# Kernel tuning notes

Measured on AMD Instinct MI355X. Metric: run time of the kernel, lower is better.

## Reference

```python
import jax, jax.numpy as jnp
import numpy as np

B, D, H, G, WR = 8192, 1024, 1024, 2, 64
URANKS = [64, 64]


def setup_inputs() -> dict:
    key = jax.random.key(0)
    ks = jax.random.split(key, 12)
    s = 0.1
    return {
        "x": jax.random.normal(ks[0], (B, D), jnp.float32),
        "h": jax.random.normal(ks[1], (B, H), jnp.float32),
        "c": jax.random.normal(ks[2], (B, H), jnp.float32),
        "dia_x": s * jax.random.normal(ks[3], (1, D), jnp.float32),
        "dia_h": s * jax.random.normal(ks[4], (1, H), jnp.float32),
        "Ux": s * jax.random.normal(ks[5], (D, WR), jnp.float32),
        "Vx": s * jax.random.normal(ks[6], (4 * H, WR), jnp.float32),
        "Uh_0": s * jax.random.normal(ks[7], (G, H // G, URANKS[0]), jnp.float32),
        "Vh_0": s * jax.random.normal(ks[8], (G, URANKS[0], 4 * (H // G)), jnp.float32),
        "Uh_1": s * jax.random.normal(ks[9], (G, H // G, URANKS[1]), jnp.float32),
        "Vh_1": s * jax.random.normal(ks[10], (G, URANKS[1], 4 * (H // G)), jnp.float32),
        "bias_x": jnp.ones((1, 4 * H), jnp.float32),
        "bias_h": jnp.ones((1, 4 * H), jnp.float32),
    }


def reference(x, h, c, dia_x, dia_h, Ux, Vx, Uh_0, Vh_0, Uh_1, Vh_1, bias_x, bias_h):
    Bn, Dn = x.shape
    Hn = h.shape[1]
    g = Uh_0.shape[0]
    Hg = Hn // g
    r0 = Uh_0.shape[2]

    # diagonal (vector-multiplication) paths, x-part zero-padded to hidden width
    vm_x = jnp.pad(dia_x * x, ((0, 0), (0, Hn - Dn)))          # [B, H]
    vm_h = dia_h * h                                           # [B, H]

    # low-rank input projection
    lowered_x = (x @ Ux) @ Vx.T                                # [B, 4H]

    # refined diagonal corrections subtracted from the low-rank outputs
    Vx4 = Vx.reshape(4, Hn, -1)[:, :Dn, :]                     # [4, D, wR]
    coef_x = jnp.sum(Ux[None, :, :] * Vx4, axis=-1)            # [4, D]
    vm_refined_x = jnp.pad(x[:, None, :] * coef_x[None], ((0, 0), (0, 0), (0, Hn - Dn))).reshape(Bn, 4 * Hn)

    Uh0f = Uh_0.reshape(Hn, r0)                                # [H, r0]
    Vh0f = jnp.transpose(Vh_0, (0, 2, 1)).reshape(4 * Hn, r0).reshape(4, Hn, r0)
    coef_h = jnp.sum(Uh0f[None, :, :] * Vh0f, axis=-1)         # [4, H]
    vm_refined_h = (h[:, None, :] * coef_h[None]).reshape(Bn, 4 * Hn)

    gx = lowered_x - vm_refined_x + bias_x
    xi, xf, xo, xn = jnp.split(gx, 4, axis=1)

    # grouped low-rank recurrent projection with cyclic group permutation
    hv = h.reshape(Bn, g, Hg)
    Uhs = [Uh_0, Uh_1]
    Vhs = [Vh_0, Vh_1]
    g_h = jnp.zeros((Bn, 4 * Hn), x.dtype)
    for i in range(g):
        idx = np.roll(np.arange(g), -i)                        # static permutation
        hp = hv[:, idx, :]                                     # [B, g, H/g]
        t = jnp.einsum('bgn,gnr->bgr', hp, Uhs[i])             # [B, g, r_i]
        t = jnp.einsum('bgr,grm->bgm', t, Vhs[i])              # [B, g, 4H/g]
        g_h = g_h + t.reshape(Bn, 4 * Hn)

    gh = g_h - vm_refined_h + bias_h
    hf, hi, hn, ho = jnp.split(gh, 4, axis=1)                  # note gate order differs from x

    base = vm_x + vm_h
    inputgate = jax.nn.sigmoid(xi + hi + base)
    forgetgate = jax.nn.sigmoid(xf + hf + base)
    outputgate = jax.nn.sigmoid(xo + ho + base)
    newgate = jnp.tanh(xn + hn + base)

    c_next = forgetgate * c + inputgate * newgate
    h_next = outputgate * jnp.tanh(c_next)
    return (h_next, c_next)
```

## Files before the change

### kernel.cpp

```cpp
#include <hip/hip_runtime.h>


typedef _Float16 half8 __attribute__((ext_vector_type(8)));
typedef _Float16 half4v __attribute__((ext_vector_type(4)));
typedef float f32x4 __attribute__((ext_vector_type(4)));

#define WS_U1F   0
#define WS_UH1F  131072
#define WS_W2    393216
#define WS_CX    1966080
#define WS_CH    1982464
#define WS_BB    1998848

__global__ __launch_bounds__(256) void prep_kernel(
    const float* __restrict__ Ux, const float* __restrict__ Vx,
    const float* __restrict__ Uh0, const float* __restrict__ Vh0,
    const float* __restrict__ Uh1, const float* __restrict__ Vh1,
    const float* __restrict__ dia_x, const float* __restrict__ dia_h,
    const float* __restrict__ bias_x, const float* __restrict__ bias_h,
    _Float16* __restrict__ U1f, _Float16* __restrict__ Uh1f,
    _Float16* __restrict__ W2f, float* __restrict__ cx,
    float* __restrict__ ch, float* __restrict__ bb)
{
    __shared__ __align__(16) _Float16 Tl[64][260];

    const int tid = threadIdx.x;
    if (blockIdx.x >= 240) {
        int bid2 = blockIdx.x - 240;
        int s = bid2 & 1, i = (bid2 >> 1) & 1, mchunk = bid2 >> 2;
        const float* Vh = i ? Vh1 : Vh0;
        #pragma unroll
        for (int it = 0; it < 16; ++it) {
            int idx = tid + it * 256;
            int row = idx >> 6, c4 = idx & 63;
            f32x4 v = *(const f32x4*)&Vh[(size_t)(s * 64 + row) * 2048
                                         + mchunk * 256 + c4 * 4];
            half4v p;
            p[0] = (_Float16)v[0]; p[1] = (_Float16)v[1];
            p[2] = (_Float16)v[2]; p[3] = (_Float16)v[3];
            *(half4v*)&Tl[row][c4 * 4] = p;
        }
        __syncthreads();
        int lane = tid & 63, l15 = lane & 15, quad = lane >> 4;
        #pragma unroll
        for (int q = 0; q < 8; ++q) {
            int combo = (tid >> 6) * 8 + q;
            int ct_local = combo >> 1, rk = combo & 1;
            int m_local = ct_local * 16 + l15;
            int m = mchunk * 256 + m_local;
            int g01 = (m >= 1024) ? 0 : 1;
            int ct_global = (m - (1 - g01) * 1024) >> 4;
            int ksq = 2 + 2 * i + rk;
            half8 v8;
            #pragma unroll
            for (int jj = 0; jj < 8; ++jj)
                v8[jj] = Tl[rk * 32 + quad * 8 + jj][m_local];
            size_t t_out = (((size_t)(s * 2 + g01) * 64 + ct_global) * 6 + ksq) * 64 + lane;
            *(half8*)&W2f[t_out * 8] = v8;
        }
        return;
    }

    int e = blockIdx.x * 256 + tid;
    if (e < 8192) {
        int lane = e & 63, ks = (e >> 6) & 31, ct = e >> 11;
        int l15 = lane & 15, quad = lane >> 4;
        half8 v8;
        #pragma unroll
        for (int jj = 0; jj < 8; ++jj) {
            int k = ks * 32 + quad * 8 + jj;
            v8[jj] = (_Float16)Ux[k * 64 + ct * 16 + l15];
        }
        *(half8*)&U1f[(size_t)e * 8] = v8;
    } else if (e < 24576) {
        int t = e - 8192;
        int lane = t & 63, ks = (t >> 6) & 15, ct = (t >> 10) & 3, j = t >> 12;
        int l15 = lane & 15, quad = lane >> 4;
        const float* src = (j & 1) ? Uh1 : Uh0;
        int g = j >> 1;
        half8 v8;
        #pragma unroll
        for (int jj = 0; jj < 8; ++jj) {
            int k = ks * 32 + quad * 8 + jj;
            v8[jj] = (_Float16)src[(g * 512 + k) * 64 + ct * 16 + l15];
        }
        *(half8*)&Uh1f[(size_t)t * 8] = v8;
    } else if (e < 57344) {
        int tt = e - 24576;
        int lane = tt & 63;
        int ksq2 = (tt >> 6) & 1;
        int ct   = (tt / 128) & 63;
        int g01  = (tt / 8192) & 1;
        int s    = tt / 16384;
        int l15 = lane & 15, quad = lane >> 4;
        int k = ct * 16 + l15;
        int jx = s * 2 + g01;
        half8 v8;
        #pragma unroll
        for (int jj = 0; jj < 8; ++jj) {
            int r = ksq2 * 32 + quad * 8 + jj;
            v8[jj] = (_Float16)Vx[(jx * 1024 + k) * 64 + r];
        }
        size_t t_out = (((size_t)(s * 2 + g01) * 64 + ct) * 6 + ksq2) * 64 + lane;
        *(half8*)&W2f[t_out * 8] = v8;
    } else if (e < 61440) {
        int t = e - 57344;
        int q = t >> 10; int k = t & 1023;
        int jh = q ^ 1;
        int fh = jh * 1024 + k; int g = fh >> 11; int m = fh & 2047;
        float sx0 = 0.f, sx1 = 0.f, sh0 = 0.f, sh1 = 0.f;
        #pragma unroll 4
        for (int r = 0; r < 64; r += 2) {
            sx0 += Ux[k * 64 + r]     * Vx[(q * 1024 + k) * 64 + r];
            sx1 += Ux[k * 64 + r + 1] * Vx[(q * 1024 + k) * 64 + r + 1];
            sh0 += Uh0[k * 64 + r]     * Vh0[(size_t)(g * 64 + r) * 2048 + m];
            sh1 += Uh0[k * 64 + r + 1] * Vh0[(size_t)(g * 64 + r + 1) * 2048 + m];
        }
        cx[t] = dia_x[k] - (sx0 + sx1);
        ch[t] = dia_h[k] - (sh0 + sh1);
        bb[t] = bias_x[q * 1024 + k] + bias_h[jh * 1024 + k];
    }
}

__global__ __launch_bounds__(1024) void fused_kernel(
    const float* __restrict__ x, const float* __restrict__ h,
    const float* __restrict__ c,
    const _Float16* __restrict__ U1f, const _Float16* __restrict__ Uh1f,
    const _Float16* __restrict__ W2f,
    const float* __restrict__ cx, const float* __restrict__ ch,
    const float* __restrict__ bb, float* __restrict__ out)
{
    __shared__ __align__(16) _Float16 Xsh[32][1032];
    __shared__ __align__(16) _Float16 Hsh[32][1032];
    __shared__ __align__(16) _Float16 Tsh[32][328];

    const int tid = threadIdx.x;
    const int w = tid >> 6, l = tid & 63, l15 = l & 15, quad = l >> 4;
    const int b0 = blockIdx.x * 32;
    const size_t rowbase = (size_t)b0 * 1024;

    {
        const float* xs = x + rowbase;
        const float* hs = h + rowbase;
        #pragma unroll
        for (int ii = 0; ii < 8; ++ii) {
            int idx = tid + ii * 1024;
            int row = idx >> 8, c4 = idx & 255;
            f32x4 fx = *(const f32x4*)&xs[(size_t)row * 1024 + c4 * 4];
            f32x4 fh = *(const f32x4*)&hs[(size_t)row * 1024 + c4 * 4];
            half4v px, ph;
            px[0] = (_Float16)fx[0]; px[1] = (_Float16)fx[1];
            px[2] = (_Float16)fx[2]; px[3] = (_Float16)fx[3];
            ph[0] = (_Float16)fh[0]; ph[1] = (_Float16)fh[1];
            ph[2] = (_Float16)fh[2]; ph[3] = (_Float16)fh[3];
            *(half4v*)&Xsh[row][c4 * 4] = px;
            *(half4v*)&Hsh[row][c4 * 4] = ph;
        }
    }
    __syncthreads();

    if (w < 8) {
        int rt = w & 1, ct = w >> 1;
        f32x4 acc = {};
        const _Float16* bp = U1f + ((size_t)(ct * 32) * 64 + l) * 8;
        #pragma unroll
        for (int ks = 0; ks < 32; ++ks) {
            half8 a = *(const half8*)&Xsh[rt * 16 + l15][ks * 32 + quad * 8];
            half8 b = *(const half8*)(bp + (size_t)ks * 512);
            acc = __builtin_amdgcn_mfma_f32_16x16x32_f16(a, b, acc, 0, 0, 0);
        }
        #pragma unroll
        for (int r = 0; r < 4; ++r)
            Tsh[rt * 16 + quad * 4 + r][ct * 16 + l15] = (_Float16)acc[r];
    }
    {
        int pstart = (w < 8) ? w : 8 + (w - 8) * 3;
        int pcnt   = (w < 8) ? 1 : 3;
        for (int ii = 0; ii < 3; ++ii) {
            if (ii >= pcnt) break;
            int p = pstart + ii;
            int j = p >> 3, rem = p & 7, prt = rem >> 2, pct = rem & 3;
            int hoff = (j == 1 || j == 2) ? 512 : 0;
            f32x4 pa = {};
            const _Float16* pb = Uh1f + ((size_t)((j * 4 + pct) * 16) * 64 + l) * 8;
            #pragma unroll
            for (int ks = 0; ks < 16; ++ks) {
                half8 a = *(const half8*)&Hsh[prt * 16 + l15][hoff + ks * 32 + quad * 8];
                half8 b = *(const half8*)(pb + (size_t)ks * 512);
                pa = __builtin_amdgcn_mfma_f32_16x16x32_f16(a, b, pa, 0, 0, 0);
            }
            #pragma unroll
            for (int r = 0; r < 4; ++r)
                Tsh[prt * 16 + quad * 4 + r][64 + j * 64 + pct * 16 + l15] = (_Float16)pa[r];
        }
    }
    __syncthreads();

    const int secIF[3] = {0, 64, 128};
    const int secON[3] = {0, 192, 256};

    float cpref[2][2][4];
    {
        int k0 = w * 16 + l15;
        #pragma unroll
        for (int rt = 0; rt < 2; ++rt)
            #pragma unroll
            for (int r = 0; r < 4; ++r)
                cpref[0][rt][r] = __builtin_nontemporal_load(
                    &c[rowbase + (size_t)(rt * 16 + quad * 4 + r) * 1024 + k0]);
    }

    #pragma unroll
    for (int i = 0; i < 4; ++i) {
        const int ctg = w + 16 * i;
        const int k = ctg * 16 + l15;

        if (i < 3) {
            int kn = k + 256;
            #pragma unroll
            for (int rt = 0; rt < 2; ++rt)
                #pragma unroll
                for (int r = 0; r < 4; ++r)
                    cpref[(i + 1) & 1][rt][r] = __builtin_nontemporal_load(
                        &c[rowbase + (size_t)(rt * 16 + quad * 4 + r) * 1024 + kn]);
        }

        float cxi = cx[k], cxf = cx[1024 + k], cxo = cx[2048 + k], cxn = cx[3072 + k];
        float chi = ch[k], chf = ch[1024 + k], cho = ch[2048 + k], chn = ch[3072 + k];
        float bbi = bb[k], bbf = bb[1024 + k], bbo = bb[2048 + k], bbn = bb[3072 + k];

        const size_t laneoff = (size_t)l * 8;
        const _Float16* bpi = W2f + (size_t)((0 * 64 + ctg) * 6) * 512 + laneoff;
        const _Float16* bpf = W2f + (size_t)((1 * 64 + ctg) * 6) * 512 + laneoff;
        const _Float16* bpo = W2f + (size_t)((2 * 64 + ctg) * 6) * 512 + laneoff;
        const _Float16* bpn = W2f + (size_t)((3 * 64 + ctg) * 6) * 512 + laneoff;

        f32x4 acc[4][2] = {};
        #pragma unroll
        for (int ks = 0; ks < 6; ++ks) {
            half8 bi = *(const half8*)(bpi + (size_t)ks * 512);
            half8 bf = *(const half8*)(bpf + (size_t)ks * 512);
            half8 bo = *(const half8*)(bpo + (size_t)ks * 512);
            half8 bn = *(const half8*)(bpn + (size_t)ks * 512);
            int coff = (ks & 1) * 32 + quad * 8;
            #pragma unroll
            for (int rt = 0; rt < 2; ++rt) {
                half8 aA = *(const half8*)&Tsh[rt * 16 + l15][secIF[ks >> 1] + coff];
                half8 aB = *(const half8*)&Tsh[rt * 16 + l15][secON[ks >> 1] + coff];
                acc[0][rt] = __builtin_amdgcn_mfma_f32_16x16x32_f16(aA, bi, acc[0][rt], 0, 0, 0);
                acc[1][rt] = __builtin_amdgcn_mfma_f32_16x16x32_f16(aA, bf, acc[1][rt], 0, 0, 0);
                acc[2][rt] = __builtin_amdgcn_mfma_f32_16x16x32_f16(aB, bo, acc[2][rt], 0, 0, 0);
                acc[3][rt] = __builtin_amdgcn_mfma_f32_16x16x32_f16(aB, bn, acc[3][rt], 0, 0, 0);
            }
        }

        #pragma unroll
        for (int rt = 0; rt < 2; ++rt) {
            #pragma unroll
            for (int r = 0; r < 4; ++r) {
                int rl = rt * 16 + quad * 4 + r;
                size_t off = rowbase + (size_t)rl * 1024 + k;
                float xv = (float)Xsh[rl][k];
                float hv = (float)Hsh[rl][k];
                float cvv = cpref[i & 1][rt][r];
                float pi = acc[0][rt][r] + xv * cxi + hv * chi + bbi;
                float pf = acc[1][rt][r] + xv * cxf + hv * chf + bbf;
                float po = acc[2][rt][r] + xv * cxo + hv * cho + bbo;
                float pn = acc[3][rt][r] + xv * cxn + hv * chn + bbn;
                float ig = __builtin_amdgcn_rcpf(1.f + __expf(-pi));
                float fg = __builtin_amdgcn_rcpf(1.f + __expf(-pf));
                float og = __builtin_amdgcn_rcpf(1.f + __expf(-po));
                float ng = 1.f - 2.f * __builtin_amdgcn_rcpf(__expf(2.f * pn) + 1.f);
                float cn = fg * cvv + ig * ng;
                float tc = 1.f - 2.f * __builtin_amdgcn_rcpf(__expf(2.f * cn) + 1.f);
                out[off] = og * tc;
                out[(size_t)8388608 + off] = cn;
            }
        }
    }
}

extern "C" void kernel_launch(void* const* d_in, const int* in_sizes, int n_in,
                              void* d_out, int out_size, void* d_ws, size_t ws_size,
                              hipStream_t stream)
{
    const float* x      = (const float*)d_in[0];
    const float* h      = (const float*)d_in[1];
    const float* c      = (const float*)d_in[2];
    const float* dia_x  = (const float*)d_in[3];
    const float* dia_h  = (const float*)d_in[4];
    const float* Ux     = (const float*)d_in[5];
    const float* Vx     = (const float*)d_in[6];
    const float* Uh0    = (const float*)d_in[7];
    const float* Vh0    = (const float*)d_in[8];
    const float* Uh1    = (const float*)d_in[9];
    const float* Vh1    = (const float*)d_in[10];
    const float* bias_x = (const float*)d_in[11];
    const float* bias_h = (const float*)d_in[12];
    float* out = (float*)d_out;

    char* ws = (char*)d_ws;
    _Float16* U1f  = (_Float16*)(ws + WS_U1F);
    _Float16* Uh1f = (_Float16*)(ws + WS_UH1F);
    _Float16* W2f  = (_Float16*)(ws + WS_W2);
    float* cx = (float*)(ws + WS_CX);
    float* ch = (float*)(ws + WS_CH);
    float* bb = (float*)(ws + WS_BB);

    prep_kernel<<<272, 256, 0, stream>>>(Ux, Vx, Uh0, Vh0, Uh1, Vh1,
                                         dia_x, dia_h, bias_x, bias_h,
                                         U1f, Uh1f, W2f, cx, ch, bb);
    fused_kernel<<<256, 1024, 0, stream>>>(x, h, c, U1f, Uh1f, W2f,
                                           cx, ch, bb, out);
}
```

Baseline: 215.0 us.

## Merge weight prep and fused LSTM kernel into one cooperative launch

Combines the weight-repacking prep kernel and the main fused LSTM-cell kernel into a single cooperative kernel with a grid-wide sync. The first blocks do the repacking while every block loads and converts its x/h tile to fp16 in shared memory, and a grid barrier separates the phases. This removes one kernel launch and lets the x/h loads overlap with weight preparation. In exchange it needs all 256 blocks of 1024 threads to be co-resident, and it adds the cost of a grid-wide barrier.

```diff
diff --git a/kernel.cpp b/kernel.cpp
--- a/kernel.cpp
+++ b/kernel.cpp
@@ -1,4 +1,7 @@
 #include <hip/hip_runtime.h>
+#include <hip/hip_cooperative_groups.h>
+
+namespace cg = cooperative_groups;
 
 
 typedef _Float16 half8 __attribute__((ext_vector_type(8)));
@@ -12,132 +15,129 @@
 #define WS_CH    1982464
 #define WS_BB    1998848
 
-__global__ __launch_bounds__(256) void prep_kernel(
+#define XSH(r,c) POOL[(r) * 1032 + (c)]
+#define HSH(r,c) POOL[33024 + (r) * 1032 + (c)]
+#define TSH(r,c) POOL[66048 + (r) * 328 + (c)]
+
+__global__ __launch_bounds__(1024) void mega_kernel(
+    const float* __restrict__ x, const float* __restrict__ h,
+    const float* __restrict__ c,
+    const float* __restrict__ dia_x, const float* __restrict__ dia_h,
     const float* __restrict__ Ux, const float* __restrict__ Vx,
     const float* __restrict__ Uh0, const float* __restrict__ Vh0,
     const float* __restrict__ Uh1, const float* __restrict__ Vh1,
-    const float* __restrict__ dia_x, const float* __restrict__ dia_h,
     const float* __restrict__ bias_x, const float* __restrict__ bias_h,
     _Float16* __restrict__ U1f, _Float16* __restrict__ Uh1f,
     _Float16* __restrict__ W2f, float* __restrict__ cx,
-    float* __restrict__ ch, float* __restrict__ bb)
+    float* __restrict__ ch, float* __restrict__ bb,
+    float* __restrict__ out)
 {
-    __shared__ __align__(16) _Float16 Tl[64][260];
+    __shared__ __align__(16) _Float16 POOL[76544];
 
     const int tid = threadIdx.x;
-    if (blockIdx.x >= 240) {
-        int bid2 = blockIdx.x - 240;
-        int s = bid2 & 1, i = (bid2 >> 1) & 1, mchunk = bid2 >> 2;
-        const float* Vh = i ? Vh1 : Vh0;
+    const int bid = blockIdx.x;
+    const int w = tid >> 6, l = tid & 63, l15 = l & 15, quad = l >> 4;
+    const int b0 = bid * 32;
+    const size_t rowbase = (size_t)b0 * 1024;
+
+    if (bid < 8) {
+        int unit = tid >> 8;
+        int ut   = tid & 255;
+        int bid2 = bid * 4 + unit;
+        _Float16* Tl = POOL + unit * 16640;
+        int s = bid2 & 1, ih = (bid2 >> 1) & 1, mchunk = bid2 >> 2;
+        const float* Vh = ih ? Vh1 : Vh0;
         #pragma unroll
         for (int it = 0; it < 16; ++it) {
-            int idx = tid + it * 256;
+            int idx = ut + it * 256;
             int row = idx >> 6, c4 = idx & 63;
             f32x4 v = *(const f32x4*)&Vh[(size_t)(s * 64 + row) * 2048
                                          + mchunk * 256 + c4 * 4];
             half4v p;
             p[0] = (_Float16)v[0]; p[1] = (_Float16)v[1];
             p[2] = (_Float16)v[2]; p[3] = (_Float16)v[3];
-            *(half4v*)&Tl[row][c4 * 4] = p;
+            *(half4v*)&Tl[row * 260 + c4 * 4] = p;
         }
         __syncthreads();
-        int lane = tid & 63, l15 = lane & 15, quad = lane >> 4;
+        int lane = ut & 63, tl15 = lane & 15, tquad = lane >> 4;
         #pragma unroll
         for (int q = 0; q < 8; ++q) {
-            int combo = (tid >> 6) * 8 + q;
+            int combo = (ut >> 6) * 8 + q;
             int ct_local = combo >> 1, rk = combo & 1;
-            int m_local = ct_local * 16 + l15;
+            int m_local = ct_local * 16 + tl15;
             int m = mchunk * 256 + m_local;
             int g01 = (m >= 1024) ? 0 : 1;
             int ct_global = (m - (1 - g01) * 1024) >> 4;
-            int ksq = 2 + 2 * i + rk;
+            int ksq = 2 + 2 * ih + rk;
             half8 v8;
             #pragma unroll
             for (int jj = 0; jj < 8; ++jj)
-                v8[jj] = Tl[rk * 32 + quad * 8 + jj][m_local];
+                v8[jj] = Tl[(rk * 32 + tquad * 8 + jj) * 260 + m_local];
             size_t t_out = (((size_t)(s * 2 + g01) * 64 + ct_global) * 6 + ksq) * 64 + lane;
             *(half8*)&W2f[t_out * 8] = v8;
         }
-        return;
-    }
-
-    int e = blockIdx.x * 256 + tid;
-    if (e < 8192) {
-        int lane = e & 63, ks = (e >> 6) & 31, ct = e >> 11;
-        int l15 = lane & 15, quad = lane >> 4;
-        half8 v8;
-        #pragma unroll
-        for (int jj = 0; jj < 8; ++jj) {
-            int k = ks * 32 + quad * 8 + jj;
-            v8[jj] = (_Float16)Ux[k * 64 + ct * 16 + l15];
-        }
-        *(half8*)&U1f[(size_t)e * 8] = v8;
-    } else if (e < 24576) {
-        int t = e - 8192;
-        int lane = t & 63, ks = (t >> 6) & 15, ct = (t >> 10) & 3, j = t >> 12;
-        int l15 = lane & 15, quad = lane >> 4;
-        const float* src = (j & 1) ? Uh1 : Uh0;
-        int g = j >> 1;
-        half8 v8;
-        #pragma unroll
-        for (int jj = 0; jj < 8; ++jj) {
-            int k = ks * 32 + quad * 8 + jj;
-            v8[jj] = (_Float16)src[(g * 512 + k) * 64 + ct * 16 + l15];
-        }
-        *(half8*)&Uh1f[(size_t)t * 8] = v8;
-    } else if (e < 57344) {
-        int tt = e - 24576;
-        int lane = tt & 63;
-        int ksq2 = (tt >> 6) & 1;
-        int ct   = (tt / 128) & 63;
-        int g01  = (tt / 8192) & 1;
-        int s    = tt / 16384;
-        int l15 = lane & 15, quad = lane >> 4;
-        int k = ct * 16 + l15;
-        int jx = s * 2 + g01;
-        half8 v8;
-        #pragma unroll
-        for (int jj = 0; jj < 8; ++jj) {
-            int r = ksq2 * 32 + quad * 8 + jj;
-            v8[jj] = (_Float16)Vx[(jx * 1024 + k) * 64 + r];
-        }
-        size_t t_out = (((size_t)(s * 2 + g01) * 64 + ct) * 6 + ksq2) * 64 + lane;
-        *(half8*)&W2f[t_out * 8] = v8;
-    } else if (e < 61440) {
-        int t = e - 57344;
-        int q = t >> 10; int k = t & 1023;
-        int jh = q ^ 1;
-        int fh = jh * 1024 + k; int g = fh >> 11; int m = fh & 2047;
-        float sx0 = 0.f, sx1 = 0.f, sh0 = 0.f, sh1 = 0.f;
-        #pragma unroll 4
-        for (int r = 0; r < 64; r += 2) {
-            sx0 += Ux[k * 64 + r]     * Vx[(q * 1024 + k) * 64 + r];
-            sx1 += Ux[k * 64 + r + 1] * Vx[(q * 1024 + k) * 64 + r + 1];
-            sh0 += Uh0[k * 64 + r]     * Vh0[(size_t)(g * 64 + r) * 2048 + m];
-            sh1 += Uh0[k * 64 + r + 1] * Vh0[(size_t)(g * 64 + r + 1) * 2048 + m];
-        }
-        cx[t] = dia_x[k] - (sx0 + sx1);
-        ch[t] = dia_h[k] - (sh0 + sh1);
-        bb[t] = bias_x[q * 1024 + k] + bias_h[jh * 1024 + k];
-    }
-}
-
-__global__ __launch_bounds__(1024) void fused_kernel(
-    const float* __restrict__ x, const float* __restrict__ h,
-    const float* __restrict__ c,
-    const _Float16* __restrict__ U1f, const _Float16* __restrict__ Uh1f,
-    const _Float16* __restrict__ W2f,
-    const float* __restrict__ cx, const float* __restrict__ ch,
-    const float* __restrict__ bb, float* __restrict__ out)
-{
-    __shared__ __align__(16) _Float16 Xsh[32][1032];
-    __shared__ __align__(16) _Float16 Hsh[32][1032];
-    __shared__ __align__(16) _Float16 Tsh[32][328];
-
-    const int tid = threadIdx.x;
-    const int w = tid >> 6, l = tid & 63, l15 = l & 15, quad = l >> 4;
-    const int b0 = blockIdx.x * 32;
-    const size_t rowbase = (size_t)b0 * 1024;
+    } else if (bid < 68) {
+        int e = (bid - 8) * 1024 + tid;
+        if (e < 8192) {
+            int lane = e & 63, ks = (e >> 6) & 31, ct = e >> 11;
+            int pl15 = lane & 15, pquad = lane >> 4;
+            half8 v8;
+            #pragma unroll
+            for (int jj = 0; jj < 8; ++jj) {
+                int k = ks * 32 + pquad * 8 + jj;
+                v8[jj] = (_Float16)Ux[k * 64 + ct * 16 + pl15];
+            }
+            *(half8*)&U1f[(size_t)e * 8] = v8;
+        } else if (e < 24576) {
+            int t = e - 8192;
+            int lane = t & 63, ks = (t >> 6) & 15, ct = (t >> 10) & 3, j = t >> 12;
+            int pl15 = lane & 15, pquad = lane >> 4;
+            const float* src = (j & 1) ? Uh1 : Uh0;
+            int g = j >> 1;
+            half8 v8;
+            #pragma unroll
+            for (int jj = 0; jj < 8; ++jj) {
+                int k = ks * 32 + pquad * 8 + jj;
+                v8[jj] = (_Float16)src[(g * 512 + k) * 64 + ct * 16 + pl15];
+            }
+            *(half8*)&Uh1f[(size_t)t * 8] = v8;
+        } else if (e < 57344) {
+            int tt = e - 24576;
+            int lane = tt & 63;
+            int ksq2 = (tt >> 6) & 1;
+            int ct   = (tt / 128) & 63;
+            int g01  = (tt / 8192) & 1;
+            int s    = tt / 16384;
+            int pl15 = lane & 15, pquad = lane >> 4;
+            int k = ct * 16 + pl15;
+            int jx = s * 2 + g01;
+            half8 v8;
+            #pragma unroll
+            for (int jj = 0; jj < 8; ++jj) {
+                int r = ksq2 * 32 + pquad * 8 + jj;
+                v8[jj] = (_Float16)Vx[(jx * 1024 + k) * 64 + r];
+            }
+            size_t t_out = (((size_t)(s * 2 + g01) * 64 + ct) * 6 + ksq2) * 64 + lane;
+            *(half8*)&W2f[t_out * 8] = v8;
+        } else {
+            int t = e - 57344;
+            int q = t >> 10; int k = t & 1023;
+            int jh = q ^ 1;
+            int fh = jh * 1024 + k; int g = fh >> 11; int m = fh & 2047;
+            float sx0 = 0.f, sx1 = 0.f, sh0 = 0.f, sh1 = 0.f;
+            #pragma unroll 4
+            for (int r = 0; r < 64; r += 2) {
+                sx0 += Ux[k * 64 + r]     * Vx[(q * 1024 + k) * 64 + r];
+                sx1 += Ux[k * 64 + r + 1] * Vx[(q * 1024 + k) * 64 + r + 1];
+                sh0 += Uh0[k * 64 + r]     * Vh0[(size_t)(g * 64 + r) * 2048 + m];
+                sh1 += Uh0[k * 64 + r + 1] * Vh0[(size_t)(g * 64 + r + 1) * 2048 + m];
+            }
+            cx[t] = dia_x[k] - (sx0 + sx1);
+            ch[t] = dia_h[k] - (sh0 + sh1);
+            bb[t] = bias_x[q * 1024 + k] + bias_h[jh * 1024 + k];
+        }
+    }
+    __syncthreads();
 
     {
         const float* xs = x + rowbase;
@@ -153,11 +153,13 @@
             px[2] = (_Float16)fx[2]; px[3] = (_Float16)fx[3];
             ph[0] = (_Float16)fh[0]; ph[1] = (_Float16)fh[1];
             ph[2] = (_Float16)fh[2]; ph[3] = (_Float16)fh[3];
-            *(half4v*)&Xsh[row][c4 * 4] = px;
-            *(half4v*)&Hsh[row][c4 * 4] = ph;
+            *(half4v*)&XSH(row, c4 * 4) = px;
+            *(half4v*)&HSH(row, c4 * 4) = ph;
         }
     }
     __syncthreads();
+
+    cg::this_grid().sync();
 
     if (w < 8) {
         int rt = w & 1, ct = w >> 1;
@@ -165,13 +167,13 @@
         const _Float16* bp = U1f + ((size_t)(ct * 32) * 64 + l) * 8;
         #pragma unroll
         for (int ks = 0; ks < 32; ++ks) {
-            half8 a = *(const half8*)&Xsh[rt * 16 + l15][ks * 32 + quad * 8];
+            half8 a = *(const half8*)&XSH(rt * 16 + l15, ks * 32 + quad * 8);
             half8 b = *(const half8*)(bp + (size_t)ks * 512);
             acc = __builtin_amdgcn_mfma_f32_16x16x32_f16(a, b, acc, 0, 0, 0);
         }
         #pragma unroll
         for (int r = 0; r < 4; ++r)
-            Tsh[rt * 16 + quad * 4 + r][ct * 16 + l15] = (_Float16)acc[r];
+            TSH(rt * 16 + quad * 4 + r, ct * 16 + l15) = (_Float16)acc[r];
     }
     {
         int pstart = (w < 8) ? w : 8 + (w - 8) * 3;
@@ -185,13 +187,13 @@
             const _Float16* pb = Uh1f + ((size_t)((j * 4 + pct) * 16) * 64 + l) * 8;
             #pragma unroll
             for (int ks = 0; ks < 16; ++ks) {
-                half8 a = *(const half8*)&Hsh[prt * 16 + l15][hoff + ks * 32 + quad * 8];
+                half8 a = *(const half8*)&HSH(prt * 16 + l15, hoff + ks * 32 + quad * 8);
                 half8 b = *(const half8*)(pb + (size_t)ks * 512);
                 pa = __builtin_amdgcn_mfma_f32_16x16x32_f16(a, b, pa, 0, 0, 0);
             }
             #pragma unroll
             for (int r = 0; r < 4; ++r)
-                Tsh[prt * 16 + quad * 4 + r][64 + j * 64 + pct * 16 + l15] = (_Float16)pa[r];
+                TSH(prt * 16 + quad * 4 + r, 64 + j * 64 + pct * 16 + l15) = (_Float16)pa[r];
         }
     }
     __syncthreads();
@@ -245,8 +247,8 @@
             int coff = (ks & 1) * 32 + quad * 8;
             #pragma unroll
             for (int rt = 0; rt < 2; ++rt) {
-                half8 aA = *(const half8*)&Tsh[rt * 16 + l15][secIF[ks >> 1] + coff];
-                half8 aB = *(const half8*)&Tsh[rt * 16 + l15][secON[ks >> 1] + coff];
+                half8 aA = *(const half8*)&TSH(rt * 16 + l15, secIF[ks >> 1] + coff);
+                half8 aB = *(const half8*)&TSH(rt * 16 + l15, secON[ks >> 1] + coff);
                 acc[0][rt] = __builtin_amdgcn_mfma_f32_16x16x32_f16(aA, bi, acc[0][rt], 0, 0, 0);
                 acc[1][rt] = __builtin_amdgcn_mfma_f32_16x16x32_f16(aA, bf, acc[1][rt], 0, 0, 0);
                 acc[2][rt] = __builtin_amdgcn_mfma_f32_16x16x32_f16(aB, bo, acc[2][rt], 0, 0, 0);
@@ -260,8 +262,8 @@
             for (int r = 0; r < 4; ++r) {
                 int rl = rt * 16 + quad * 4 + r;
                 size_t off = rowbase + (size_t)rl * 1024 + k;
-                float xv = (float)Xsh[rl][k];
-                float hv = (float)Hsh[rl][k];
+                float xv = (float)XSH(rl, k);
+                float hv = (float)HSH(rl, k);
                 float cvv = cpref[i & 1][rt][r];
                 float pi = acc[0][rt][r] + xv * cxi + hv * chi + bbi;
                 float pf = acc[1][rt][r] + xv * cxf + hv * chf + bbf;
@@ -303,13 +305,20 @@
     _Float16* U1f  = (_Float16*)(ws + WS_U1F);
     _Float16* Uh1f = (_Float16*)(ws + WS_UH1F);
     _Float16* W2f  = (_Float16*)(ws + WS_W2);
-    float* cx = (float*)(ws + WS_CX);
-    float* ch = (float*)(ws + WS_CH);
-    float* bb = (float*)(ws + WS_BB);
-
-    prep_kernel<<<272, 256, 0, stream>>>(Ux, Vx, Uh0, Vh0, Uh1, Vh1,
-                                         dia_x, dia_h, bias_x, bias_h,
-                                         U1f, Uh1f, W2f, cx, ch, bb);
-    fused_kernel<<<256, 1024, 0, stream>>>(x, h, c, U1f, Uh1f, W2f,
-                                           cx, ch, bb, out);
+    float* cxp = (float*)(ws + WS_CX);
+    float* chp = (float*)(ws + WS_CH);
+    float* bbp = (float*)(ws + WS_BB);
+
+    void* args[] = {
+        (void*)&x, (void*)&h, (void*)&c,
+        (void*)&dia_x, (void*)&dia_h,
+        (void*)&Ux, (void*)&Vx,
+        (void*)&Uh0, (void*)&Vh0, (void*)&Uh1, (void*)&Vh1,
+        (void*)&bias_x, (void*)&bias_h,
+        (void*)&U1f, (void*)&Uh1f, (void*)&W2f,
+        (void*)&cxp, (void*)&chp, (void*)&bbp,
+        (void*)&out
+    };
+    hipLaunchCooperativeKernel((void*)mega_kernel, dim3(256), dim3(1024),
+                               args, 0, stream);
 }
```

Result: slower. 327.8 us (+52.4%).
